# Optimization experiments

Hardware: AMD Instinct MI355X
Metric: run time of the kernel (lower is better)

The kernel has to match this reference:

```python
import jax, jax.numpy as jnp
import numpy as np
import math

HEAD = 4

def _neighbors3x3(t):
    # t: [b, g, d, h, w] -> [b, g, d, 9, h, w], zero-padded 3x3 neighborhoods
    b, g, d, h, w = t.shape
    tp = jnp.pad(t, ((0, 0), (0, 0), (0, 0), (1, 1), (1, 1)))
    # torch.nn.Unfold(kernel_size=3) ordering: kernel positions row-major (dy, dx)
    patches = [tp[:, :, :, dy:dy + h, dx:dx + w] for dy in range(3) for dx in range(3)]
    return jnp.stack(patches, axis=3)


def setup_inputs() -> dict:
    key = jax.random.key(0)
    k1, k2 = jax.random.split(key)
    x = jax.random.normal(k1, (8, 128, 96, 96), dtype=jnp.float32)
    # 1x1 conv weight, no bias: [out=3*out_features, in=in_features]
    W_trans = jax.random.normal(k2, (384, 128), dtype=jnp.float32) * 0.05
    return {"x": x, "W_trans": W_trans}


def reference(x, W_trans):
    b, cin, h, w = x.shape
    # 1x1 conv == channel GEMM
    t = jnp.einsum('bchw,oc->bohw', x, W_trans)  # [b, 3*C, h, w]
    q, k, v = jnp.split(t, 3, axis=1)            # each [b, C, h, w]
    C = q.shape[1]
    d = C // HEAD
    q = q.reshape(b, HEAD, d, h, w)
    k = k.reshape(b, HEAD, d, h, w)
    v = v.reshape(b, HEAD, d, h, w)
    kn = _neighbors3x3(k)  # [b, g, d, 9, h, w]
    vn = _neighbors3x3(v)  # [b, g, d, 9, h, w]
    # att[b,g,n,h,w] = <q[b,g,:,h,w], kn[b,g,:,n,h,w]> / sqrt(d)
    att = jnp.einsum('bgdhw,bgdnhw->bgnhw', q, kn) / math.sqrt(d)
    att = jax.nn.softmax(att, axis=2)
    # dropout p=0.4 is identity in eval mode
    out = jnp.einsum('bgnhw,bgdnhw->bgdhw', att, vn)  # [b, g, d, h, w]
    return out.reshape(b, C, h, w)
```

## Files before the change

kernel.cpp:

```cpp
#include <hip/hip_runtime.h>

#define NB     8
#define CIN    128
#define HEADS  4
#define DHEAD  32
#define HDIM   96
#define WDIM   96
#define HW     9216

#define TH     8
#define TW     16
#define HR     (TH + 2)
#define HC     (TW + 2)
#define HP     (HR * HC)
#define NT     12
#define NPOS   (NT * 16)
#define NPOSP  (NPOS + 1)

typedef __bf16 bf16x8 __attribute__((ext_vector_type(8)));
typedef float  f32x4  __attribute__((ext_vector_type(4)));

__device__ __forceinline__ unsigned f2bf(float f) {
  unsigned u = __float_as_uint(f);
  return (u + 0x7fffu + ((u >> 16) & 1u)) >> 16;
}
__device__ __forceinline__ unsigned pack2(float a, float b) {
  return f2bf(a) | (f2bf(b) << 16);
}
__device__ __forceinline__ float bflo(unsigned u) { return __uint_as_float(u << 16); }
__device__ __forceinline__ float bfhi(unsigned u) { return __uint_as_float(u & 0xffff0000u); }

__global__ __launch_bounds__(256) void wpack_kernel(const float* __restrict__ W,
                                                    uint4* __restrict__ Wf) {
  const int u = blockIdx.x * 256 + threadIdx.x;
  const int lane = u & 63, kb = (u >> 6) & 3, ot = u >> 8;
  const int o = ot * 16 + (lane & 15);
  const int c0 = kb * 32 + (lane >> 4) * 8;
  const float4* w = (const float4*)(W + (size_t)o * CIN + c0);
  float4 w0 = w[0], w1 = w[1];
  uint4 r;
  r.x = pack2(w0.x, w0.y); r.y = pack2(w0.z, w0.w);
  r.z = pack2(w1.x, w1.y); r.w = pack2(w1.z, w1.w);
  Wf[u] = r;
}

__global__ __launch_bounds__(128) void fused_kernel(const float* __restrict__ x,
                                                    const uint4* __restrict__ Wf,
                                                    float* __restrict__ out) {
  __shared__ uint4 qs[4 * NPOSP];
  __shared__ uint4 ks[4 * NPOSP];
  __shared__ uint4 vs[4 * NPOSP];

  const int b  = blockIdx.z;
  const int h0 = blockIdx.y * TH;
  const int w0 = blockIdx.x * TW;
  const int t  = threadIdx.x;
  const int wv = t >> 6, lane = t & 63;
  const int colp = lane & 15, quad = lane >> 4;

  uint4 frags[6][4];
  {
    const size_t xbase = (size_t)b * CIN * HW;
#pragma unroll
    for (int i = 0; i < 6; ++i) {
      const int tt = wv * 6 + i;
      const int hp = tt * 16 + colp;
      const int hr = hp / HC, hc = hp - hr * HC;
      const int hh = h0 - 1 + hr, ww = w0 - 1 + hc;
      const bool ok = (hp < HP) & (hh >= 0) & (hh < HDIM) & (ww >= 0) & (ww < WDIM);
#pragma unroll
      for (int kb = 0; kb < 4; ++kb) {
        const int c0 = kb * 32 + quad * 8;
        float f[8] = {0.f, 0.f, 0.f, 0.f, 0.f, 0.f, 0.f, 0.f};
        if (ok) {
          const size_t pbyte = xbase + (size_t)(hh * WDIM + ww);
#pragma unroll
          for (int j = 0; j < 8; ++j) f[j] = x[pbyte + (size_t)(c0 + j) * HW];
        }
        uint4 r;
        r.x = pack2(f[0], f[1]); r.y = pack2(f[2], f[3]);
        r.z = pack2(f[4], f[5]); r.w = pack2(f[6], f[7]);
        frags[i][kb] = r;
      }
    }
  }

  const int y  = t >> 4, xx = t & 15;
  const int pbase = (y + 1) * HC + (xx + 1);

#pragma unroll 1
  for (int g = 0; g < 4; ++g) {
    if (g) __syncthreads();

#pragma unroll
    for (int s = 0; s < 3; ++s) {
      uint4* dst = (s == 0) ? qs : (s == 1) ? ks : vs;
#pragma unroll
      for (int ph = 0; ph < 2; ++ph) {
        const int ot = s * 8 + g * 2 + ph;
        bf16x8 af[4];
#pragma unroll
        for (int kb = 0; kb < 4; ++kb) {
          uint4 tmp = Wf[(ot * 4 + kb) * 64 + lane];
          af[kb] = *(bf16x8*)&tmp;
        }
        const int d0 = ph * 16 + quad * 4;
        const int c = d0 >> 3, sub = (d0 >> 2) & 1;
#pragma unroll
        for (int i = 0; i < 6; ++i) {
          f32x4 acc = {0.f, 0.f, 0.f, 0.f};
#pragma unroll
          for (int kb = 0; kb < 4; ++kb)
            acc = __builtin_amdgcn_mfma_f32_16x16x32_bf16(
                af[kb], *(bf16x8*)&frags[i][kb], acc, 0, 0, 0);
          uint2 st;
          st.x = pack2(acc[0], acc[1]);
          st.y = pack2(acc[2], acc[3]);
          const int pos = (wv * 6 + i) * 16 + colp;
          *(uint2*)((unsigned short*)(dst + c * NPOSP + pos) + sub * 4) = st;
        }
      }
    }
    __syncthreads();

    float q[32];
#pragma unroll
    for (int c = 0; c < 4; ++c) {
      uint4 u = qs[c * NPOSP + pbase];
      q[c * 8 + 0] = bflo(u.x); q[c * 8 + 1] = bfhi(u.x);
      q[c * 8 + 2] = bflo(u.y); q[c * 8 + 3] = bfhi(u.y);
      q[c * 8 + 4] = bflo(u.z); q[c * 8 + 5] = bfhi(u.z);
      q[c * 8 + 6] = bflo(u.w); q[c * 8 + 7] = bfhi(u.w);
    }

    float att[9];
#pragma unroll
    for (int nn = 0; nn < 9; ++nn) {
      const int pn = pbase + (nn / 3 - 1) * HC + (nn % 3 - 1);
      float dot = 0.0f;
#pragma unroll
      for (int c = 0; c < 4; ++c) {
        uint4 u = ks[c * NPOSP + pn];
        dot = fmaf(q[c * 8 + 0], bflo(u.x), dot);
        dot = fmaf(q[c * 8 + 1], bfhi(u.x), dot);
        dot = fmaf(q[c * 8 + 2], bflo(u.y), dot);
        dot = fmaf(q[c * 8 + 3], bfhi(u.y), dot);
        dot = fmaf(q[c * 8 + 4], bflo(u.z), dot);
        dot = fmaf(q[c * 8 + 5], bfhi(u.z), dot);
        dot = fmaf(q[c * 8 + 6], bflo(u.w), dot);
        dot = fmaf(q[c * 8 + 7], bfhi(u.w), dot);
      }
      att[nn] = dot * 0.17677669529663687f;
    }

    float m = att[0];
#pragma unroll
    for (int nn = 1; nn < 9; ++nn) m = fmaxf(m, att[nn]);
    float s = 0.0f;
#pragma unroll
    for (int nn = 0; nn < 9; ++nn) { att[nn] = __expf(att[nn] - m); s += att[nn]; }
    const float inv = 1.0f / s;

    float acc[32];
#pragma unroll
    for (int i = 0; i < 32; ++i) acc[i] = 0.0f;
#pragma unroll
    for (int nn = 0; nn < 9; ++nn) {
      const float wn = att[nn] * inv;
      const int pn = pbase + (nn / 3 - 1) * HC + (nn % 3 - 1);
#pragma unroll
      for (int c = 0; c < 4; ++c) {
        uint4 u = vs[c * NPOSP + pn];
        acc[c * 8 + 0] = fmaf(wn, bflo(u.x), acc[c * 8 + 0]);
        acc[c * 8 + 1] = fmaf(wn, bfhi(u.x), acc[c * 8 + 1]);
        acc[c * 8 + 2] = fmaf(wn, bflo(u.y), acc[c * 8 + 2]);
        acc[c * 8 + 3] = fmaf(wn, bfhi(u.y), acc[c * 8 + 3]);
        acc[c * 8 + 4] = fmaf(wn, bflo(u.z), acc[c * 8 + 4]);
        acc[c * 8 + 5] = fmaf(wn, bfhi(u.z), acc[c * 8 + 5]);
        acc[c * 8 + 6] = fmaf(wn, bflo(u.w), acc[c * 8 + 6]);
        acc[c * 8 + 7] = fmaf(wn, bfhi(u.w), acc[c * 8 + 7]);
      }
    }

    float* ob = out + ((size_t)b * CIN + (size_t)g * DHEAD) * HW
              + (size_t)(h0 + y) * WDIM + (w0 + xx);
#pragma unroll
    for (int i = 0; i < 32; ++i) ob[(size_t)i * HW] = acc[i];
  }
}

extern "C" void kernel_launch(void* const* d_in, const int* in_sizes, int n_in,
                              void* d_out, int out_size, void* d_ws, size_t ws_size,
                              hipStream_t stream) {
  (void)in_sizes; (void)n_in; (void)out_size; (void)ws_size;
  const float* x = (const float*)d_in[0];
  const float* W = (const float*)d_in[1];
  float* out = (float*)d_out;

  uint4* Wf = (uint4*)d_ws;

  wpack_kernel<<<24, 256, 0, stream>>>(W, Wf);
  fused_kernel<<<dim3(WDIM / TW, HDIM / TH, NB), 128, 0, stream>>>(x, Wf, out);
}
```

Measured before the change: 139.0 us.

## Split heads across blocks instead of looping per block

Moves the head loop into the grid z dimension so each block handles one head, giving four times as many blocks for occupancy. Each block now reloads the x halo tile from global memory, so total x reads grow fourfold. Q storage is trimmed to the interior pixels only and the padded stride is removed, which cuts shared memory but may add LDS bank conflicts.

Measured after the change: 159.7 us. 1.15x slower.

```diff
diff --git a/kernel.cpp b/kernel.cpp
--- a/kernel.cpp
+++ b/kernel.cpp
@@ -15,7 +15,7 @@
 #define HP     (HR * HC)
 #define NT     12
 #define NPOS   (NT * 16)
-#define NPOSP  (NPOS + 1)
+#define QP     (TH * TW)
 
 typedef __bf16 bf16x8 __attribute__((ext_vector_type(8)));
 typedef float  f32x4  __attribute__((ext_vector_type(4)));
@@ -47,11 +47,12 @@
 __global__ __launch_bounds__(128) void fused_kernel(const float* __restrict__ x,
                                                     const uint4* __restrict__ Wf,
                                                     float* __restrict__ out) {
-  __shared__ uint4 qs[4 * NPOSP];
-  __shared__ uint4 ks[4 * NPOSP];
-  __shared__ uint4 vs[4 * NPOSP];
-
-  const int b  = blockIdx.z;
+  __shared__ uint4 qs[4 * QP];
+  __shared__ uint4 ks[4 * NPOS];
+  __shared__ uint4 vs[4 * NPOS];
+
+  const int z  = blockIdx.z;
+  const int b  = z >> 2, g = z & 3;
   const int h0 = blockIdx.y * TH;
   const int w0 = blockIdx.x * TW;
   const int t  = threadIdx.x;
@@ -63,8 +64,7 @@
     const size_t xbase = (size_t)b * CIN * HW;
 #pragma unroll
     for (int i = 0; i < 6; ++i) {
-      const int tt = wv * 6 + i;
-      const int hp = tt * 16 + colp;
+      const int hp = (wv * 6 + i) * 16 + colp;
       const int hr = hp / HC, hc = hp - hr * HC;
       const int hh = h0 - 1 + hr, ww = w0 - 1 + hc;
       const bool ok = (hp < HP) & (hh >= 0) & (hh < HDIM) & (ww >= 0) & (ww < WDIM);
@@ -85,108 +85,111 @@
     }
   }
 
-  const int y  = t >> 4, xx = t & 15;
-  const int pbase = (y + 1) * HC + (xx + 1);
-
-#pragma unroll 1
-  for (int g = 0; g < 4; ++g) {
-    if (g) __syncthreads();
-
-#pragma unroll
-    for (int s = 0; s < 3; ++s) {
-      uint4* dst = (s == 0) ? qs : (s == 1) ? ks : vs;
-#pragma unroll
-      for (int ph = 0; ph < 2; ++ph) {
-        const int ot = s * 8 + g * 2 + ph;
-        bf16x8 af[4];
-#pragma unroll
-        for (int kb = 0; kb < 4; ++kb) {
-          uint4 tmp = Wf[(ot * 4 + kb) * 64 + lane];
-          af[kb] = *(bf16x8*)&tmp;
-        }
-        const int d0 = ph * 16 + quad * 4;
-        const int c = d0 >> 3, sub = (d0 >> 2) & 1;
-#pragma unroll
-        for (int i = 0; i < 6; ++i) {
-          f32x4 acc = {0.f, 0.f, 0.f, 0.f};
-#pragma unroll
-          for (int kb = 0; kb < 4; ++kb)
-            acc = __builtin_amdgcn_mfma_f32_16x16x32_bf16(
-                af[kb], *(bf16x8*)&frags[i][kb], acc, 0, 0, 0);
-          uint2 st;
-          st.x = pack2(acc[0], acc[1]);
-          st.y = pack2(acc[2], acc[3]);
-          const int pos = (wv * 6 + i) * 16 + colp;
-          *(uint2*)((unsigned short*)(dst + c * NPOSP + pos) + sub * 4) = st;
+#pragma unroll
+  for (int s = 0; s < 3; ++s) {
+#pragma unroll
+    for (int ph = 0; ph < 2; ++ph) {
+      const int ot = s * 8 + g * 2 + ph;
+      bf16x8 af[4];
+#pragma unroll
+      for (int kb = 0; kb < 4; ++kb) {
+        uint4 tmp = Wf[(ot * 4 + kb) * 64 + lane];
+        af[kb] = *(bf16x8*)&tmp;
+      }
+      const int d0 = ph * 16 + quad * 4;
+      const int c = d0 >> 3, sub = (d0 >> 2) & 1;
+#pragma unroll
+      for (int i = 0; i < 6; ++i) {
+        f32x4 acc = {0.f, 0.f, 0.f, 0.f};
+#pragma unroll
+        for (int kb = 0; kb < 4; ++kb)
+          acc = __builtin_amdgcn_mfma_f32_16x16x32_bf16(
+              af[kb], *(bf16x8*)&frags[i][kb], acc, 0, 0, 0);
+        uint2 st;
+        st.x = pack2(acc[0], acc[1]);
+        st.y = pack2(acc[2], acc[3]);
+        const int pos = (wv * 6 + i) * 16 + colp;
+        if (s == 0) {
+          const int hr = pos / HC, hc = pos - hr * HC;
+          if (((unsigned)(hr - 1) < TH) & ((unsigned)(hc - 1) < TW)) {
+            const int idx = (hr - 1) * TW + (hc - 1);
+            *(uint2*)((unsigned short*)(qs + c * QP + idx) + sub * 4) = st;
+          }
+        } else {
+          uint4* dst = (s == 1) ? ks : vs;
+          *(uint2*)((unsigned short*)(dst + c * NPOS + pos) + sub * 4) = st;
         }
       }
     }
-    __syncthreads();
-
-    float q[32];
+  }
+  __syncthreads();
+
+  const int y = t >> 4, xx = t & 15;
+  const int pbase = (y + 1) * HC + (xx + 1);
+
+  float q[32];
+#pragma unroll
+  for (int c = 0; c < 4; ++c) {
+    uint4 u = qs[c * QP + t];
+    q[c * 8 + 0] = bflo(u.x); q[c * 8 + 1] = bfhi(u.x);
+    q[c * 8 + 2] = bflo(u.y); q[c * 8 + 3] = bfhi(u.y);
+    q[c * 8 + 4] = bflo(u.z); q[c * 8 + 5] = bfhi(u.z);
+    q[c * 8 + 6] = bflo(u.w); q[c * 8 + 7] = bfhi(u.w);
+  }
+
+  float att[9];
+#pragma unroll
+  for (int nn = 0; nn < 9; ++nn) {
+    const int pn = pbase + (nn / 3 - 1) * HC + (nn % 3 - 1);
+    float dot = 0.0f;
 #pragma unroll
     for (int c = 0; c < 4; ++c) {
-      uint4 u = qs[c * NPOSP + pbase];
-      q[c * 8 + 0] = bflo(u.x); q[c * 8 + 1] = bfhi(u.x);
-      q[c * 8 + 2] = bflo(u.y); q[c * 8 + 3] = bfhi(u.y);
-      q[c * 8 + 4] = bflo(u.z); q[c * 8 + 5] = bfhi(u.z);
-      q[c * 8 + 6] = bflo(u.w); q[c * 8 + 7] = bfhi(u.w);
-    }
-
-    float att[9];
-#pragma unroll
-    for (int nn = 0; nn < 9; ++nn) {
-      const int pn = pbase + (nn / 3 - 1) * HC + (nn % 3 - 1);
-      float dot = 0.0f;
-#pragma unroll
-      for (int c = 0; c < 4; ++c) {
-        uint4 u = ks[c * NPOSP + pn];
-        dot = fmaf(q[c * 8 + 0], bflo(u.x), dot);
-        dot = fmaf(q[c * 8 + 1], bfhi(u.x), dot);
-        dot = fmaf(q[c * 8 + 2], bflo(u.y), dot);
-        dot = fmaf(q[c * 8 + 3], bfhi(u.y), dot);
-        dot = fmaf(q[c * 8 + 4], bflo(u.z), dot);
-        dot = fmaf(q[c * 8 + 5], bfhi(u.z), dot);
-        dot = fmaf(q[c * 8 + 6], bflo(u.w), dot);
-        dot = fmaf(q[c * 8 + 7], bfhi(u.w), dot);
-      }
-      att[nn] = dot * 0.17677669529663687f;
-    }
-
-    float m = att[0];
-#pragma unroll
-    for (int nn = 1; nn < 9; ++nn) m = fmaxf(m, att[nn]);
-    float s = 0.0f;
-#pragma unroll
-    for (int nn = 0; nn < 9; ++nn) { att[nn] = __expf(att[nn] - m); s += att[nn]; }
-    const float inv = 1.0f / s;
-
-    float acc[32];
-#pragma unroll
-    for (int i = 0; i < 32; ++i) acc[i] = 0.0f;
-#pragma unroll
-    for (int nn = 0; nn < 9; ++nn) {
-      const float wn = att[nn] * inv;
-      const int pn = pbase + (nn / 3 - 1) * HC + (nn % 3 - 1);
-#pragma unroll
-      for (int c = 0; c < 4; ++c) {
-        uint4 u = vs[c * NPOSP + pn];
-        acc[c * 8 + 0] = fmaf(wn, bflo(u.x), acc[c * 8 + 0]);
-        acc[c * 8 + 1] = fmaf(wn, bfhi(u.x), acc[c * 8 + 1]);
-        acc[c * 8 + 2] = fmaf(wn, bflo(u.y), acc[c * 8 + 2]);
-        acc[c * 8 + 3] = fmaf(wn, bfhi(u.y), acc[c * 8 + 3]);
-        acc[c * 8 + 4] = fmaf(wn, bflo(u.z), acc[c * 8 + 4]);
-        acc[c * 8 + 5] = fmaf(wn, bfhi(u.z), acc[c * 8 + 5]);
-        acc[c * 8 + 6] = fmaf(wn, bflo(u.w), acc[c * 8 + 6]);
-        acc[c * 8 + 7] = fmaf(wn, bfhi(u.w), acc[c * 8 + 7]);
-      }
-    }
-
-    float* ob = out + ((size_t)b * CIN + (size_t)g * DHEAD) * HW
-              + (size_t)(h0 + y) * WDIM + (w0 + xx);
-#pragma unroll
-    for (int i = 0; i < 32; ++i) ob[(size_t)i * HW] = acc[i];
-  }
+      uint4 u = ks[c * NPOS + pn];
+      dot = fmaf(q[c * 8 + 0], bflo(u.x), dot);
+      dot = fmaf(q[c * 8 + 1], bfhi(u.x), dot);
+      dot = fmaf(q[c * 8 + 2], bflo(u.y), dot);
+      dot = fmaf(q[c * 8 + 3], bfhi(u.y), dot);
+      dot = fmaf(q[c * 8 + 4], bflo(u.z), dot);
+      dot = fmaf(q[c * 8 + 5], bfhi(u.z), dot);
+      dot = fmaf(q[c * 8 + 6], bflo(u.w), dot);
+      dot = fmaf(q[c * 8 + 7], bfhi(u.w), dot);
+    }
+    att[nn] = dot * 0.17677669529663687f;
+  }
+
+  float m = att[0];
+#pragma unroll
+  for (int nn = 1; nn < 9; ++nn) m = fmaxf(m, att[nn]);
+  float s = 0.0f;
+#pragma unroll
+  for (int nn = 0; nn < 9; ++nn) { att[nn] = __expf(att[nn] - m); s += att[nn]; }
+  const float inv = 1.0f / s;
+
+  float acc[32];
+#pragma unroll
+  for (int i = 0; i < 32; ++i) acc[i] = 0.0f;
+#pragma unroll
+  for (int nn = 0; nn < 9; ++nn) {
+    const float wn = att[nn] * inv;
+    const int pn = pbase + (nn / 3 - 1) * HC + (nn % 3 - 1);
+#pragma unroll
+    for (int c = 0; c < 4; ++c) {
+      uint4 u = vs[c * NPOS + pn];
+      acc[c * 8 + 0] = fmaf(wn, bflo(u.x), acc[c * 8 + 0]);
+      acc[c * 8 + 1] = fmaf(wn, bfhi(u.x), acc[c * 8 + 1]);
+      acc[c * 8 + 2] = fmaf(wn, bflo(u.y), acc[c * 8 + 2]);
+      acc[c * 8 + 3] = fmaf(wn, bfhi(u.y), acc[c * 8 + 3]);
+      acc[c * 8 + 4] = fmaf(wn, bflo(u.z), acc[c * 8 + 4]);
+      acc[c * 8 + 5] = fmaf(wn, bfhi(u.z), acc[c * 8 + 5]);
+      acc[c * 8 + 6] = fmaf(wn, bflo(u.w), acc[c * 8 + 6]);
+      acc[c * 8 + 7] = fmaf(wn, bfhi(u.w), acc[c * 8 + 7]);
+    }
+  }
+
+  float* ob = out + ((size_t)b * CIN + (size_t)g * DHEAD) * HW
+            + (size_t)(h0 + y) * WDIM + (w0 + xx);
+#pragma unroll
+  for (int i = 0; i < 32; ++i) ob[(size_t)i * HW] = acc[i];
 }
 
 extern "C" void kernel_launch(void* const* d_in, const int* in_sizes, int n_in,
@@ -200,5 +203,5 @@
   uint4* Wf = (uint4*)d_ws;
 
   wpack_kernel<<<24, 256, 0, stream>>>(W, Wf);
-  fused_kernel<<<dim3(WDIM / TW, HDIM / TH, NB), 128, 0, stream>>>(x, Wf, out);
-}
+  fused_kernel<<<dim3(WDIM / TW, HDIM / TH, NB * HEADS), 128, 0, stream>>>(x, Wf, out);
+}
```

## Switch to fp16 MFMA with dot2, 256-thread blocks splitting head dims

Applied to the files above, without the earlier changes.

Block size doubles to 256 threads. Each wave now projects 3 halo tiles instead of 6, and in the attention phase each pair of threads splits the 32 head channels of one output pixel in half. Precision moves from bf16 to fp16 using cvt_pkrtz and the packed fdot2 instruction, which cuts unpack/FMA work in the QK dot product. V is kept in fp32 in shared memory so the weighted sum needs no unpacking, and Q is stored only for the interior pixels. The split duplicates the QK dot and softmax in both threads of a pair, uses more LDS for fp32 V, and fp16 with round-toward-zero carries some range and accuracy risk.

Result: faster. 129.9 us (-6.6%).

```diff
diff --git a/kernel.cpp b/kernel.cpp
--- a/kernel.cpp
+++ b/kernel.cpp
@@ -16,19 +16,25 @@
 #define NT     12
 #define NPOS   (NT * 16)
 #define NPOSP  (NPOS + 1)
-
-typedef __bf16 bf16x8 __attribute__((ext_vector_type(8)));
-typedef float  f32x4  __attribute__((ext_vector_type(4)));
-
-__device__ __forceinline__ unsigned f2bf(float f) {
-  unsigned u = __float_as_uint(f);
-  return (u + 0x7fffu + ((u >> 16) & 1u)) >> 16;
-}
-__device__ __forceinline__ unsigned pack2(float a, float b) {
-  return f2bf(a) | (f2bf(b) << 16);
-}
-__device__ __forceinline__ float bflo(unsigned u) { return __uint_as_float(u << 16); }
-__device__ __forceinline__ float bfhi(unsigned u) { return __uint_as_float(u & 0xffff0000u); }
+#define QP     (TH * TW)
+
+typedef __fp16 f16x2 __attribute__((ext_vector_type(2)));
+typedef __fp16 f16x8 __attribute__((ext_vector_type(8)));
+typedef float  f32x4 __attribute__((ext_vector_type(4)));
+
+__device__ __forceinline__ unsigned pkh2(float a, float b) {
+  f16x2 h = __builtin_amdgcn_cvt_pkrtz(a, b);
+  return *(unsigned*)&h;
+}
+__device__ __forceinline__ float dot2(unsigned a, unsigned b, float c) {
+#if __has_builtin(__builtin_amdgcn_fdot2)
+  return __builtin_amdgcn_fdot2(*(f16x2*)&a, *(f16x2*)&b, c, false);
+#else
+  f16x2 ha = *(f16x2*)&a, hb = *(f16x2*)&b;
+  c = fmaf((float)ha[0], (float)hb[0], c);
+  return fmaf((float)ha[1], (float)hb[1], c);
+#endif
+}
 
 __global__ __launch_bounds__(256) void wpack_kernel(const float* __restrict__ W,
                                                     uint4* __restrict__ Wf) {
@@ -39,17 +45,17 @@
   const float4* w = (const float4*)(W + (size_t)o * CIN + c0);
   float4 w0 = w[0], w1 = w[1];
   uint4 r;
-  r.x = pack2(w0.x, w0.y); r.y = pack2(w0.z, w0.w);
-  r.z = pack2(w1.x, w1.y); r.w = pack2(w1.z, w1.w);
+  r.x = pkh2(w0.x, w0.y); r.y = pkh2(w0.z, w0.w);
+  r.z = pkh2(w1.x, w1.y); r.w = pkh2(w1.z, w1.w);
   Wf[u] = r;
 }
 
-__global__ __launch_bounds__(128) void fused_kernel(const float* __restrict__ x,
+__global__ __launch_bounds__(256) void fused_kernel(const float* __restrict__ x,
                                                     const uint4* __restrict__ Wf,
                                                     float* __restrict__ out) {
-  __shared__ uint4 qs[4 * NPOSP];
+  __shared__ uint4 qs[4 * QP];
   __shared__ uint4 ks[4 * NPOSP];
-  __shared__ uint4 vs[4 * NPOSP];
+  __shared__ f32x4 vs[8 * NPOSP];
 
   const int b  = blockIdx.z;
   const int h0 = blockIdx.y * TH;
@@ -58,13 +64,12 @@
   const int wv = t >> 6, lane = t & 63;
   const int colp = lane & 15, quad = lane >> 4;
 
-  uint4 frags[6][4];
+  uint4 frags[3][4];
   {
     const size_t xbase = (size_t)b * CIN * HW;
 #pragma unroll
-    for (int i = 0; i < 6; ++i) {
-      const int tt = wv * 6 + i;
-      const int hp = tt * 16 + colp;
+    for (int i = 0; i < 3; ++i) {
+      const int hp = (wv * 3 + i) * 16 + colp;
       const int hr = hp / HC, hc = hp - hr * HC;
       const int hh = h0 - 1 + hr, ww = w0 - 1 + hc;
       const bool ok = (hp < HP) & (hh >= 0) & (hh < HDIM) & (ww >= 0) & (ww < WDIM);
@@ -73,19 +78,20 @@
         const int c0 = kb * 32 + quad * 8;
         float f[8] = {0.f, 0.f, 0.f, 0.f, 0.f, 0.f, 0.f, 0.f};
         if (ok) {
-          const size_t pbyte = xbase + (size_t)(hh * WDIM + ww);
-#pragma unroll
-          for (int j = 0; j < 8; ++j) f[j] = x[pbyte + (size_t)(c0 + j) * HW];
+          const size_t pb = xbase + (size_t)(hh * WDIM + ww);
+#pragma unroll
+          for (int j = 0; j < 8; ++j) f[j] = x[pb + (size_t)(c0 + j) * HW];
         }
         uint4 r;
-        r.x = pack2(f[0], f[1]); r.y = pack2(f[2], f[3]);
-        r.z = pack2(f[4], f[5]); r.w = pack2(f[6], f[7]);
+        r.x = pkh2(f[0], f[1]); r.y = pkh2(f[2], f[3]);
+        r.z = pkh2(f[4], f[5]); r.w = pkh2(f[6], f[7]);
         frags[i][kb] = r;
       }
     }
   }
 
-  const int y  = t >> 4, xx = t & 15;
+  const int pos = t & 127, dh = t >> 7;
+  const int y = pos >> 4, xx = pos & 15;
   const int pbase = (y + 1) * HC + (xx + 1);
 
 #pragma unroll 1
@@ -94,43 +100,53 @@
 
 #pragma unroll
     for (int s = 0; s < 3; ++s) {
-      uint4* dst = (s == 0) ? qs : (s == 1) ? ks : vs;
 #pragma unroll
       for (int ph = 0; ph < 2; ++ph) {
         const int ot = s * 8 + g * 2 + ph;
-        bf16x8 af[4];
+        f16x8 af[4];
 #pragma unroll
         for (int kb = 0; kb < 4; ++kb) {
           uint4 tmp = Wf[(ot * 4 + kb) * 64 + lane];
-          af[kb] = *(bf16x8*)&tmp;
+          af[kb] = *(f16x8*)&tmp;
         }
         const int d0 = ph * 16 + quad * 4;
-        const int c = d0 >> 3, sub = (d0 >> 2) & 1;
-#pragma unroll
-        for (int i = 0; i < 6; ++i) {
+#pragma unroll
+        for (int i = 0; i < 3; ++i) {
           f32x4 acc = {0.f, 0.f, 0.f, 0.f};
 #pragma unroll
           for (int kb = 0; kb < 4; ++kb)
-            acc = __builtin_amdgcn_mfma_f32_16x16x32_bf16(
-                af[kb], *(bf16x8*)&frags[i][kb], acc, 0, 0, 0);
-          uint2 st;
-          st.x = pack2(acc[0], acc[1]);
-          st.y = pack2(acc[2], acc[3]);
-          const int pos = (wv * 6 + i) * 16 + colp;
-          *(uint2*)((unsigned short*)(dst + c * NPOSP + pos) + sub * 4) = st;
+            acc = __builtin_amdgcn_mfma_f32_16x16x32_f16(
+                af[kb], *(f16x8*)&frags[i][kb], acc, 0, 0, 0);
+          const int pw = (wv * 3 + i) * 16 + colp;
+          if (s == 2) {
+            vs[(d0 >> 2) * NPOSP + pw] = acc;
+          } else {
+            uint2 st;
+            st.x = pkh2(acc[0], acc[1]);
+            st.y = pkh2(acc[2], acc[3]);
+            if (s == 0) {
+              const int hr = pw / HC, hc = pw - hr * HC;
+              if (((unsigned)(hr - 1) < TH) & ((unsigned)(hc - 1) < TW)) {
+                const int idx = (hr - 1) * TW + (hc - 1);
+                *(uint2*)((unsigned short*)(qs + (d0 >> 3) * QP + idx)
+                          + ((d0 >> 2) & 1) * 4) = st;
+              }
+            } else {
+              *(uint2*)((unsigned short*)(ks + (d0 >> 3) * NPOSP + pw)
+                        + ((d0 >> 2) & 1) * 4) = st;
+            }
+          }
         }
       }
     }
     __syncthreads();
 
-    float q[32];
+    unsigned qp[16];
 #pragma unroll
     for (int c = 0; c < 4; ++c) {
-      uint4 u = qs[c * NPOSP + pbase];
-      q[c * 8 + 0] = bflo(u.x); q[c * 8 + 1] = bfhi(u.x);
-      q[c * 8 + 2] = bflo(u.y); q[c * 8 + 3] = bfhi(u.y);
-      q[c * 8 + 4] = bflo(u.z); q[c * 8 + 5] = bfhi(u.z);
-      q[c * 8 + 6] = bflo(u.w); q[c * 8 + 7] = bfhi(u.w);
+      uint4 u = qs[c * QP + pos];
+      qp[c * 4 + 0] = u.x; qp[c * 4 + 1] = u.y;
+      qp[c * 4 + 2] = u.z; qp[c * 4 + 3] = u.w;
     }
 
     float att[9];
@@ -140,15 +156,11 @@
       float dot = 0.0f;
 #pragma unroll
       for (int c = 0; c < 4; ++c) {
-        uint4 u = ks[c * NPOSP + pn];
-        dot = fmaf(q[c * 8 + 0], bflo(u.x), dot);
-        dot = fmaf(q[c * 8 + 1], bfhi(u.x), dot);
-        dot = fmaf(q[c * 8 + 2], bflo(u.y), dot);
-        dot = fmaf(q[c * 8 + 3], bfhi(u.y), dot);
-        dot = fmaf(q[c * 8 + 4], bflo(u.z), dot);
-        dot = fmaf(q[c * 8 + 5], bfhi(u.z), dot);
-        dot = fmaf(q[c * 8 + 6], bflo(u.w), dot);
-        dot = fmaf(q[c * 8 + 7], bfhi(u.w), dot);
+        uint4 ku = ks[c * NPOSP + pn];
+        dot = dot2(qp[c * 4 + 0], ku.x, dot);
+        dot = dot2(qp[c * 4 + 1], ku.y, dot);
+        dot = dot2(qp[c * 4 + 2], ku.z, dot);
+        dot = dot2(qp[c * 4 + 3], ku.w, dot);
       }
       att[nn] = dot * 0.17677669529663687f;
     }
@@ -156,36 +168,32 @@
     float m = att[0];
 #pragma unroll
     for (int nn = 1; nn < 9; ++nn) m = fmaxf(m, att[nn]);
-    float s = 0.0f;
-#pragma unroll
-    for (int nn = 0; nn < 9; ++nn) { att[nn] = __expf(att[nn] - m); s += att[nn]; }
-    const float inv = 1.0f / s;
-
-    float acc[32];
-#pragma unroll
-    for (int i = 0; i < 32; ++i) acc[i] = 0.0f;
+    float ssum = 0.0f;
+#pragma unroll
+    for (int nn = 0; nn < 9; ++nn) { att[nn] = __expf(att[nn] - m); ssum += att[nn]; }
+    const float inv = 1.0f / ssum;
+
+    f32x4 acc4[4];
+#pragma unroll
+    for (int j = 0; j < 4; ++j) acc4[j] = (f32x4){0.f, 0.f, 0.f, 0.f};
 #pragma unroll
     for (int nn = 0; nn < 9; ++nn) {
       const float wn = att[nn] * inv;
       const int pn = pbase + (nn / 3 - 1) * HC + (nn % 3 - 1);
 #pragma unroll
-      for (int c = 0; c < 4; ++c) {
-        uint4 u = vs[c * NPOSP + pn];
-        acc[c * 8 + 0] = fmaf(wn, bflo(u.x), acc[c * 8 + 0]);
-        acc[c * 8 + 1] = fmaf(wn, bfhi(u.x), acc[c * 8 + 1]);
-        acc[c * 8 + 2] = fmaf(wn, bflo(u.y), acc[c * 8 + 2]);
-        acc[c * 8 + 3] = fmaf(wn, bfhi(u.y), acc[c * 8 + 3]);
-        acc[c * 8 + 4] = fmaf(wn, bflo(u.z), acc[c * 8 + 4]);
-        acc[c * 8 + 5] = fmaf(wn, bfhi(u.z), acc[c * 8 + 5]);
-        acc[c * 8 + 6] = fmaf(wn, bflo(u.w), acc[c * 8 + 6]);
-        acc[c * 8 + 7] = fmaf(wn, bfhi(u.w), acc[c * 8 + 7]);
-      }
-    }
-
-    float* ob = out + ((size_t)b * CIN + (size_t)g * DHEAD) * HW
+      for (int j = 0; j < 4; ++j) {
+        f32x4 vv = vs[(dh * 4 + j) * NPOSP + pn];
+        acc4[j] += wn * vv;
+      }
+    }
+
+    float* ob = out + ((size_t)b * CIN + (size_t)g * DHEAD + (size_t)dh * 16) * HW
               + (size_t)(h0 + y) * WDIM + (w0 + xx);
 #pragma unroll
-    for (int i = 0; i < 32; ++i) ob[(size_t)i * HW] = acc[i];
+    for (int j = 0; j < 4; ++j)
+#pragma unroll
+      for (int e = 0; e < 4; ++e)
+        ob[(size_t)(j * 4 + e) * HW] = acc4[j][e];
   }
 }
 
@@ -200,5 +208,5 @@
   uint4* Wf = (uint4*)d_ws;
 
   wpack_kernel<<<24, 256, 0, stream>>>(W, Wf);
-  fused_kernel<<<dim3(WDIM / TW, HDIM / TH, NB), 128, 0, stream>>>(x, Wf, out);
-}
+  fused_kernel<<<dim3(WDIM / TW, HDIM / TH, NB), 256, 0, stream>>>(x, Wf, out);
+}
```
